# Optimization experiments

Hardware: AMD Instinct MI355X
Metric: run time of the kernel (lower is better)

The kernel has to match this reference:

```python
import jax, jax.numpy as jnp
import numpy as np


def setup_inputs() -> dict:
    key = jax.random.key(0)
    ks = jax.random.split(key, 4)
    b, n, d, dp = 8, 4096, 256, 512
    X = jax.random.normal(ks[0], (b, n, d), dtype=jnp.float32)
    P = jax.random.normal(ks[1], (b, n, d), dtype=jnp.float32)
    # linear hypernetwork params (Kaiming-ish scale)
    Wh1 = jax.random.normal(ks[2], (d, dp), dtype=jnp.float32) * (1.0 / np.sqrt(d))
    Wh2 = jax.random.normal(ks[3], (d, dp), dtype=jnp.float32) * (1.0 / np.sqrt(d))
    bh1 = jnp.zeros((dp,), dtype=jnp.float32)
    bh2 = jnp.zeros((dp,), dtype=jnp.float32)
    return {"X": X, "P": P, "Wh1": Wh1, "bh1": bh1, "Wh2": Wh2, "bh2": bh2}


def reference(X, P, Wh1, bh1, Wh2, bh2):
    # X, P: [b, n, d]
    Xp = X + P
    # hypernetwork-generated per-sample mixing weights: [b, n, d_prime]
    W1 = Xp @ Wh1 + bh1
    W2 = Xp @ Wh2 + bh2
    # token mixing: project tokens down to d_prime "mixing" space, GELU, back up
    Pm = jnp.einsum('bnp,bnd->bpd', W1, Xp)           # [b, d_prime, d]
    A = jax.nn.gelu(Pm, approximate=False)             # torch nn.GELU is exact erf form
    Y = jnp.einsum('bnp,bpd->bnd', W2, A)              # [b, n, d]
    return Y
```

## Files before the change

kernel.cpp:

```cpp
#include <hip/hip_runtime.h>

#define DEV static __device__ __forceinline__

typedef unsigned short u16;
typedef __bf16 bf16_t;
typedef __bf16 bf16x8 __attribute__((ext_vector_type(8)));
typedef float f32x4 __attribute__((ext_vector_type(4)));
typedef u16 u16x8 __attribute__((ext_vector_type(8)));

static constexpr int Bb = 8;
static constexpr int Nn = 4096;
static constexpr int Dd = 256;
static constexpr int DP = 512;

DEV void gload16(const void* g, void* l) {
  __builtin_amdgcn_global_load_lds(
      (__attribute__((address_space(1))) void*)(unsigned long long)(g),
      (__attribute__((address_space(3))) void*)(unsigned)(unsigned long long)(l),
      16, 0, 0);
}

DEV u16 f2bf(float x) { bf16_t h = (bf16_t)x; return __builtin_bit_cast(u16, h); }
DEV float bf2f(u16 v) { unsigned u = ((unsigned)v) << 16; return __builtin_bit_cast(float, u); }
DEV float gelu_exact(float x) { return 0.5f * x * (1.0f + erff(x * 0.70710678118654752f)); }

DEV void gemm_tile(const u16* Ag, int lda, const u16* Bg, int ldb,
                   int k0, int ksteps, u16* ldsA, u16* ldsB, f32x4 acc[4][4]) {
  const int tid  = threadIdx.x;
  const int wave = tid >> 6, lane = tid & 63;
  const int wr = wave >> 1, wc = wave & 1;
  const int lr = lane & 15, lk = (lane >> 4) * 8;
  const int srow = lane >> 2;
  const int skb  = (lane & 3) * 8;
  const int c0 = wave * 2, c1 = c0 + 1;
  const size_t ga0 = (size_t)(c0 * 16 + srow) * lda + skb;
  const size_t ga1 = (size_t)(c1 * 16 + srow) * lda + skb;
  const size_t gb0 = (size_t)(c0 * 16 + srow) * ldb + skb;
  const size_t gb1 = (size_t)(c1 * 16 + srow) * ldb + skb;
  u16* la0 = ldsA + c0 * 512; u16* la1 = ldsA + c1 * 512;
  u16* lb0 = ldsB + c0 * 512; u16* lb1 = ldsB + c1 * 512;

  gload16(Ag + ga0 + k0, la0); gload16(Ag + ga1 + k0, la1);
  gload16(Bg + gb0 + k0, lb0); gload16(Bg + gb1 + k0, lb1);
  asm volatile("s_waitcnt vmcnt(0)" ::: "memory");
  __syncthreads();

  int cur = 0;
  for (int kt = 0; kt < ksteps; ++kt) {
    const int nbuf = cur ^ 1;
    if (kt + 1 < ksteps) {
      const int kk = k0 + (kt + 1) * 32;
      gload16(Ag + ga0 + kk, la0 + nbuf * 4096);
      gload16(Ag + ga1 + kk, la1 + nbuf * 4096);
      gload16(Bg + gb0 + kk, lb0 + nbuf * 4096);
      gload16(Bg + gb1 + kk, lb1 + nbuf * 4096);
    }
    const u16* pa = ldsA + cur * 4096;
    const u16* pb = ldsB + cur * 4096;
    bf16x8 af[4], bfr[4];
#pragma unroll
    for (int m = 0; m < 4; ++m)
      af[m] = *(const bf16x8*)(pa + (wr * 64 + m * 16 + lr) * 32 + lk);
#pragma unroll
    for (int n = 0; n < 4; ++n)
      bfr[n] = *(const bf16x8*)(pb + (wc * 64 + n * 16 + lr) * 32 + lk);
#pragma unroll
    for (int m = 0; m < 4; ++m)
#pragma unroll
      for (int n = 0; n < 4; ++n)
        acc[m][n] = __builtin_amdgcn_mfma_f32_16x16x32_bf16(af[m], bfr[n], acc[m][n], 0, 0, 0);
    asm volatile("s_waitcnt vmcnt(0)" ::: "memory");
    __syncthreads();
    cur = nbuf;
  }
}

DEV void acc_zero(f32x4 acc[4][4]) {
#pragma unroll
  for (int m = 0; m < 4; ++m)
#pragma unroll
    for (int n = 0; n < 4; ++n) {
      f32x4 z = {0.f, 0.f, 0.f, 0.f};
      acc[m][n] = z;
    }
}

__global__ __launch_bounds__(256) void k_s1(const float* __restrict__ X, const float* __restrict__ P,
                                            const float* __restrict__ Wh1, const float* __restrict__ Wh2,
                                            u16* __restrict__ Xp, u16* __restrict__ XpT,
                                            float* __restrict__ s_part,
                                            u16* __restrict__ WhT1, u16* __restrict__ Wbf2) {
  __shared__ u16 lt[64 * 65];
  const int bid = blockIdx.x;
  const int t = threadIdx.x;
  if (bid < 2048) {
    const int b  = bid >> 8;
    const int nt = (bid >> 2) & 63;
    const int dt = bid & 3;
    const int n0 = nt * 64, d0 = dt * 64;
    const int r = t >> 2, c0 = (t & 3) * 16;
    const size_t gbase = ((size_t)(b * Nn + n0 + r)) * Dd + d0 + c0;
    u16x8 lo, hi;
#pragma unroll
    for (int i = 0; i < 4; ++i) {
      float4 xv = *(const float4*)(X + gbase + i * 4);
      float4 pv = *(const float4*)(P + gbase + i * 4);
      u16 a0 = f2bf(xv.x + pv.x), a1 = f2bf(xv.y + pv.y);
      u16 a2 = f2bf(xv.z + pv.z), a3 = f2bf(xv.w + pv.w);
      if (i < 2) { lo[i*4+0]=a0; lo[i*4+1]=a1; lo[i*4+2]=a2; lo[i*4+3]=a3; }
      else       { int q=(i-2)*4; hi[q+0]=a0; hi[q+1]=a1; hi[q+2]=a2; hi[q+3]=a3; }
      lt[r * 65 + c0 + i*4 + 0] = a0; lt[r * 65 + c0 + i*4 + 1] = a1;
      lt[r * 65 + c0 + i*4 + 2] = a2; lt[r * 65 + c0 + i*4 + 3] = a3;
    }
    *(u16x8*)(Xp + gbase)     = lo;
    *(u16x8*)(Xp + gbase + 8) = hi;
    __syncthreads();
    const int dd = t >> 2, nc0 = (t & 3) * 16;
    u16x8 olo, ohi;
    float colsum = 0.f;
#pragma unroll
    for (int i = 0; i < 8; ++i) { olo[i] = lt[(nc0 + i) * 65 + dd]; colsum += bf2f(olo[i]); }
#pragma unroll
    for (int i = 0; i < 8; ++i) { ohi[i] = lt[(nc0 + 8 + i) * 65 + dd]; colsum += bf2f(ohi[i]); }
    const size_t obase = ((size_t)(b * Dd + d0 + dd)) * Nn + n0 + nc0;
    *(u16x8*)(XpT + obase)     = olo;
    *(u16x8*)(XpT + obase + 8) = ohi;
    colsum += __shfl_xor(colsum, 1);
    colsum += __shfl_xor(colsum, 2);
    if ((t & 3) == 0) s_part[(size_t)(b * 64 + nt) * Dd + d0 + dd] = colsum;
  } else if (bid < 2048 + 32) {
    const int wb = bid - 2048;
    const int rt = (wb >> 3) & 3;
    const int ct = wb & 7;
    const int r0 = rt * 64, c0t = ct * 64;
    const int r = t >> 2, c0 = (t & 3) * 16;
    const size_t gbase = (size_t)(r0 + r) * DP + c0t + c0;
#pragma unroll
    for (int i = 0; i < 4; ++i) {
      float4 v = *(const float4*)(Wh1 + gbase + i * 4);
      lt[r * 65 + c0 + i*4 + 0] = f2bf(v.x); lt[r * 65 + c0 + i*4 + 1] = f2bf(v.y);
      lt[r * 65 + c0 + i*4 + 2] = f2bf(v.z); lt[r * 65 + c0 + i*4 + 3] = f2bf(v.w);
    }
    __syncthreads();
    const int pp = t >> 2, dc0 = (t & 3) * 16;
    u16x8 olo, ohi;
#pragma unroll
    for (int i = 0; i < 8; ++i) olo[i] = lt[(dc0 + i) * 65 + pp];
#pragma unroll
    for (int i = 0; i < 8; ++i) ohi[i] = lt[(dc0 + 8 + i) * 65 + pp];
    u16* out = WhT1 + (size_t)(c0t + pp) * Dd + r0 + dc0;
    *(u16x8*)(out)     = olo;
    *(u16x8*)(out + 8) = ohi;
  } else {
    const int idx = ((bid - 2048 - 32) * 256 + t) * 8;
    float4 v0 = *(const float4*)(Wh2 + idx);
    float4 v1 = *(const float4*)(Wh2 + idx + 4);
    u16x8 o;
    o[0]=f2bf(v0.x); o[1]=f2bf(v0.y); o[2]=f2bf(v0.z); o[3]=f2bf(v0.w);
    o[4]=f2bf(v1.x); o[5]=f2bf(v1.y); o[6]=f2bf(v1.z); o[7]=f2bf(v1.w);
    *(u16x8*)(Wbf2 + idx) = o;
  }
}

__global__ __launch_bounds__(256) void k_gram(const u16* __restrict__ XpT, float* __restrict__ G_part) {
  __shared__ __align__(16) u16 ldsA[2 * 128 * 32];
  __shared__ __align__(16) u16 ldsB[2 * 128 * 32];
  const int bid0 = blockIdx.x;
  const int bid = (bid0 & 7) * 32 + (bid0 >> 3);
  const int kc = bid & 7;
  const int tn = (bid >> 3) & 1;
  const int tm = (bid >> 4) & 1;
  const int b  = bid >> 5;
  const u16* Ag = XpT + (size_t)(b * Dd + tm * 128) * Nn;
  const u16* Bg = XpT + (size_t)(b * Dd + tn * 128) * Nn;
  f32x4 acc[4][4];
  acc_zero(acc);
  gemm_tile(Ag, Nn, Bg, Nn, kc * 512, 16, ldsA, ldsB, acc);
  const int tid = threadIdx.x, wave = tid >> 6, lane = tid & 63;
  const int wr = wave >> 1, wc = wave & 1, lr = lane & 15, lq = lane >> 4;
  float* base = G_part + (size_t)kc * (Bb * Dd * Dd) + (size_t)(b * Dd + tm * 128) * Dd + tn * 128;
#pragma unroll
  for (int m = 0; m < 4; ++m)
#pragma unroll
    for (int n = 0; n < 4; ++n)
#pragma unroll
      for (int j = 0; j < 4; ++j)
        base[(size_t)(wr * 64 + m * 16 + lq * 4 + j) * Dd + wc * 64 + n * 16 + lr] = acc[m][n][j];
}

__global__ __launch_bounds__(256) void k_gsum(const float* __restrict__ G_part,
                                              const float* __restrict__ s_part,
                                              u16* __restrict__ Gb, float* __restrict__ s,
                                              float* __restrict__ c) {
  const int bid = blockIdx.x;
  const int t = threadIdx.x;
  if (bid < 8) {
    const int b = bid, d = t;
    float sum = 0.f;
#pragma unroll 8
    for (int nt = 0; nt < 64; ++nt) sum += s_part[(size_t)(b * 64 + nt) * Dd + d];
    s[b * Dd + d] = sum;
    c[b * Dd + d] = 0.f;
  } else {
    const int e = ((bid - 8) * 256 + t) * 8;
    float4 a0 = {0.f,0.f,0.f,0.f}, a1 = {0.f,0.f,0.f,0.f};
#pragma unroll
    for (int k = 0; k < 8; ++k) {
      const float* sp = G_part + (size_t)k * (Bb * Dd * Dd) + e;
      float4 v0 = *(const float4*)(sp);
      float4 v1 = *(const float4*)(sp + 4);
      a0.x += v0.x; a0.y += v0.y; a0.z += v0.z; a0.w += v0.w;
      a1.x += v1.x; a1.y += v1.y; a1.z += v1.z; a1.w += v1.w;
    }
    u16x8 o;
    o[0]=f2bf(a0.x); o[1]=f2bf(a0.y); o[2]=f2bf(a0.z); o[3]=f2bf(a0.w);
    o[4]=f2bf(a1.x); o[5]=f2bf(a1.y); o[6]=f2bf(a1.z); o[7]=f2bf(a1.w);
    *(u16x8*)(Gb + e) = o;
  }
}

__global__ __launch_bounds__(256) void k_pmAT(const u16* __restrict__ WhT1, const u16* __restrict__ Gb,
                                              const float* __restrict__ bh1, const float* __restrict__ s,
                                              const float* __restrict__ bh2,
                                              u16* __restrict__ AT, float* __restrict__ c) {
  __shared__ __align__(16) u16 ldsA[2 * 128 * 32];
  __shared__ __align__(16) u16 ldsB[2 * 128 * 32];
  __shared__ __align__(16) u16 ct[128 * 136];
  const int bid = blockIdx.x;
  const int tn = bid & 1;
  const int tm = (bid >> 1) & 3;
  const int b  = bid >> 3;
  const int p0 = tm * 128, d0 = tn * 128;
  const u16* Ag = WhT1 + (size_t)p0 * Dd;
  const u16* Bg = Gb + (size_t)(b * Dd + d0) * Dd;
  f32x4 acc[4][4];
  acc_zero(acc);
  gemm_tile(Ag, Dd, Bg, Dd, 0, Dd / 32, ldsA, ldsB, acc);
  const int tid = threadIdx.x, wave = tid >> 6, lane = tid & 63;
  const int wr = wave >> 1, wc = wave & 1, lr = lane & 15, lq = lane >> 4;
#pragma unroll
  for (int n = 0; n < 4; ++n) {
    const int col = wc * 64 + n * 16 + lr;
    const float sv = s[b * Dd + d0 + col];
#pragma unroll
    for (int m = 0; m < 4; ++m) {
#pragma unroll
      for (int j = 0; j < 4; ++j) {
        const int row = wr * 64 + m * 16 + lq * 4 + j;
        const float pm = acc[m][n][j] + bh1[p0 + row] * sv;
        ct[col * 136 + row] = f2bf(gelu_exact(pm));
      }
    }
  }
  __syncthreads();
#pragma unroll
  for (int it = 0; it < 8; ++it) {
    const int id = tid + it * 256;
    const int dl = id >> 4, ch = id & 15;
    *(u16x8*)(AT + (size_t)(b * Dd + d0 + dl) * DP + p0 + ch * 8) =
        *(const u16x8*)(ct + dl * 136 + ch * 8);
  }
  const int ccol = tid >> 1;
  const int chalf = tid & 1;
  float csum = 0.f;
#pragma unroll
  for (int q = 0; q < 8; ++q) {
    u16x8 av = *(const u16x8*)(ct + ccol * 136 + chalf * 64 + q * 8);
#pragma unroll
    for (int i = 0; i < 8; ++i) csum += bh2[p0 + chalf * 64 + q * 8 + i] * bf2f(av[i]);
  }
  csum += __shfl_xor(csum, 1);
  if (chalf == 0) atomicAdd(c + b * Dd + d0 + ccol, csum);
}

__global__ __launch_bounds__(256) void k_h(const u16* __restrict__ Wbf2, const u16* __restrict__ AT,
                                           u16* __restrict__ HT) {
  __shared__ __align__(16) u16 ldsA[2 * 128 * 32];
  __shared__ __align__(16) u16 ldsB[2 * 128 * 32];
  __shared__ __align__(16) u16 ct[128 * 136];
  const int bid = blockIdx.x;
  const int tn = bid & 1;
  const int tm = (bid >> 1) & 1;
  const int b  = bid >> 2;
  const int k0 = tm * 128, d0 = tn * 128;
  const u16* Ag = Wbf2 + (size_t)k0 * DP;
  const u16* Bg = AT + (size_t)(b * Dd + d0) * DP;
  f32x4 acc[4][4];
  acc_zero(acc);
  gemm_tile(Ag, DP, Bg, DP, 0, DP / 32, ldsA, ldsB, acc);
  const int tid = threadIdx.x, wave = tid >> 6, lane = tid & 63;
  const int wr = wave >> 1, wc = wave & 1, lr = lane & 15, lq = lane >> 4;
#pragma unroll
  for (int n = 0; n < 4; ++n) {
    const int col = wc * 64 + n * 16 + lr;
#pragma unroll
    for (int m = 0; m < 4; ++m)
#pragma unroll
      for (int j = 0; j < 4; ++j)
        ct[col * 136 + wr * 64 + m * 16 + lq * 4 + j] = f2bf(acc[m][n][j]);
  }
  __syncthreads();
#pragma unroll
  for (int it = 0; it < 8; ++it) {
    const int id = tid + it * 256;
    const int dl = id >> 4, ch = id & 15;
    *(u16x8*)(HT + (size_t)(b * Dd + d0 + dl) * Dd + k0 + ch * 8) =
        *(const u16x8*)(ct + dl * 136 + ch * 8);
  }
}

__global__ __launch_bounds__(256) void k_y(const u16* __restrict__ Xp, const u16* __restrict__ HT,
                                           const float* __restrict__ c, float* __restrict__ Y) {
  __shared__ __align__(16) u16 ldsA[2 * 128 * 32];
  __shared__ __align__(16) u16 ldsB[2 * 128 * 32];
  const int bid0 = blockIdx.x;
  const int bid = (bid0 & 7) * 64 + (bid0 >> 3);
  const int tn = bid & 1;
  const int tm = (bid >> 1) & 31;
  const int b  = bid >> 6;
  const u16* Ag = Xp + (size_t)(b * Nn + tm * 128) * Dd;
  const u16* Bg = HT + (size_t)(b * Dd + tn * 128) * Dd;
  f32x4 acc[4][4];
  acc_zero(acc);
  gemm_tile(Ag, Dd, Bg, Dd, 0, Dd / 32, ldsA, ldsB, acc);
  const int tid = threadIdx.x, wave = tid >> 6, lane = tid & 63;
  const int wr = wave >> 1, wc = wave & 1, lr = lane & 15, lq = lane >> 4;
  float* base = Y + (size_t)(b * Nn + tm * 128) * Dd + tn * 128;
#pragma unroll
  for (int n = 0; n < 4; ++n) {
    const int col = wc * 64 + n * 16 + lr;
    const float cv = c[b * Dd + tn * 128 + col];
#pragma unroll
    for (int m = 0; m < 4; ++m)
#pragma unroll
      for (int j = 0; j < 4; ++j)
        base[(size_t)(wr * 64 + m * 16 + lq * 4 + j) * Dd + col] = acc[m][n][j] + cv;
  }
}

extern "C" void kernel_launch(void* const* d_in, const int* in_sizes, int n_in,
                              void* d_out, int out_size, void* d_ws, size_t ws_size,
                              hipStream_t stream) {
  const float* X   = (const float*)d_in[0];
  const float* P   = (const float*)d_in[1];
  const float* Wh1 = (const float*)d_in[2];
  const float* bh1 = (const float*)d_in[3];
  const float* Wh2 = (const float*)d_in[4];
  const float* bh2 = (const float*)d_in[5];
  float* Y = (float*)d_out;
  char* ws = (char*)d_ws;

  u16*   Xp     = (u16*)(ws);
  u16*   XpT    = (u16*)(ws + 16777216);
  u16*   WhT1   = (u16*)(ws + 33554432);
  u16*   Wbf2   = (u16*)(ws + 33816576);
  float* G_part = (float*)(ws + 34078720);
  float* s_part = (float*)(ws + 50855936);
  float* s      = (float*)(ws + 51380224);
  float* c      = (float*)(ws + 51388416);
  u16*   Gb     = (u16*)(ws + 51396608);
  u16*   AT     = (u16*)(ws + 52445184);
  u16*   HT     = (u16*)(ws + 54542336);
  const size_t WS_NEED = 55590912;
  if (ws_size < WS_NEED) return;

  k_s1  <<<2144, 256, 0, stream>>>(X, P, Wh1, Wh2, Xp, XpT, s_part, WhT1, Wbf2);
  k_gram<<<256,  256, 0, stream>>>(XpT, G_part);
  k_gsum<<<264,  256, 0, stream>>>(G_part, s_part, Gb, s, c);
  k_pmAT<<<64,   256, 0, stream>>>(WhT1, Gb, bh1, s, bh2, AT, c);
  k_h   <<<32,   256, 0, stream>>>(Wbf2, AT, HT);
  k_y   <<<512,  256, 0, stream>>>(Xp, HT, c, Y);
}
```

Measured before the change: 74.44 us.

## Replace split-K Gram partials and reduction kernel with atomic accumulation into fp32 G

The Gram kernel now accumulates its split-K results straight into a single fp32 G buffer with atomicAdd, and G is zeroed by extra blocks in the first kernel. This removes the separate k_gsum kernel and the 16 MB partial buffer round trip. k_pmAT reads the fp32 G directly, converts it to bf16 while loading fragments, and reduces s_part itself. It drops a launch and a lot of memory traffic, but adds atomic contention, makes the sum order nondeterministic, and uses a simpler single-buffered load loop in k_pmAT.

```diff
diff --git a/kernel.cpp b/kernel.cpp
--- a/kernel.cpp
+++ b/kernel.cpp
@@ -89,7 +89,8 @@
                                             const float* __restrict__ Wh1, const float* __restrict__ Wh2,
                                             u16* __restrict__ Xp, u16* __restrict__ XpT,
                                             float* __restrict__ s_part,
-                                            u16* __restrict__ WhT1, u16* __restrict__ Wbf2) {
+                                            u16* __restrict__ WhT1, u16* __restrict__ Wbf2,
+                                            float* __restrict__ G) {
   __shared__ u16 lt[64 * 65];
   const int bid = blockIdx.x;
   const int t = threadIdx.x;
@@ -151,7 +152,7 @@
     u16* out = WhT1 + (size_t)(c0t + pp) * Dd + r0 + dc0;
     *(u16x8*)(out)     = olo;
     *(u16x8*)(out + 8) = ohi;
-  } else {
+  } else if (bid < 2048 + 32 + 64) {
     const int idx = ((bid - 2048 - 32) * 256 + t) * 8;
     float4 v0 = *(const float4*)(Wh2 + idx);
     float4 v1 = *(const float4*)(Wh2 + idx + 4);
@@ -159,13 +160,24 @@
     o[0]=f2bf(v0.x); o[1]=f2bf(v0.y); o[2]=f2bf(v0.z); o[3]=f2bf(v0.w);
     o[4]=f2bf(v1.x); o[5]=f2bf(v1.y); o[6]=f2bf(v1.z); o[7]=f2bf(v1.w);
     *(u16x8*)(Wbf2 + idx) = o;
-  }
-}
-
-__global__ __launch_bounds__(256) void k_gram(const u16* __restrict__ XpT, float* __restrict__ G_part) {
+  } else {
+    const int idx = ((bid - 2144) * 256 + t) * 8;
+    float4 z = {0.f, 0.f, 0.f, 0.f};
+    *(float4*)(G + idx)     = z;
+    *(float4*)(G + idx + 4) = z;
+  }
+}
+
+__global__ __launch_bounds__(256) void k_gram(const u16* __restrict__ XpT, float* __restrict__ G,
+                                              float* __restrict__ c) {
   __shared__ __align__(16) u16 ldsA[2 * 128 * 32];
   __shared__ __align__(16) u16 ldsB[2 * 128 * 32];
   const int bid0 = blockIdx.x;
+  const int tid = threadIdx.x;
+  if (bid0 >= 256) {
+    c[(bid0 - 256) * Dd + tid] = 0.f;
+    return;
+  }
   const int bid = (bid0 & 7) * 32 + (bid0 >> 3);
   const int kc = bid & 7;
   const int tn = (bid >> 3) & 1;
@@ -176,78 +188,95 @@
   f32x4 acc[4][4];
   acc_zero(acc);
   gemm_tile(Ag, Nn, Bg, Nn, kc * 512, 16, ldsA, ldsB, acc);
-  const int tid = threadIdx.x, wave = tid >> 6, lane = tid & 63;
+  const int wave = tid >> 6, lane = tid & 63;
   const int wr = wave >> 1, wc = wave & 1, lr = lane & 15, lq = lane >> 4;
-  float* base = G_part + (size_t)kc * (Bb * Dd * Dd) + (size_t)(b * Dd + tm * 128) * Dd + tn * 128;
+  float* base = G + (size_t)(b * Dd + tm * 128) * Dd + tn * 128;
 #pragma unroll
   for (int m = 0; m < 4; ++m)
 #pragma unroll
     for (int n = 0; n < 4; ++n)
 #pragma unroll
       for (int j = 0; j < 4; ++j)
-        base[(size_t)(wr * 64 + m * 16 + lq * 4 + j) * Dd + wc * 64 + n * 16 + lr] = acc[m][n][j];
-}
-
-__global__ __launch_bounds__(256) void k_gsum(const float* __restrict__ G_part,
+        atomicAdd(base + (size_t)(wr * 64 + m * 16 + lq * 4 + j) * Dd + wc * 64 + n * 16 + lr,
+                  acc[m][n][j]);
+}
+
+__global__ __launch_bounds__(256) void k_pmAT(const u16* __restrict__ WhT1, const float* __restrict__ G,
                                               const float* __restrict__ s_part,
-                                              u16* __restrict__ Gb, float* __restrict__ s,
-                                              float* __restrict__ c) {
-  const int bid = blockIdx.x;
-  const int t = threadIdx.x;
-  if (bid < 8) {
-    const int b = bid, d = t;
-    float sum = 0.f;
-#pragma unroll 8
-    for (int nt = 0; nt < 64; ++nt) sum += s_part[(size_t)(b * 64 + nt) * Dd + d];
-    s[b * Dd + d] = sum;
-    c[b * Dd + d] = 0.f;
-  } else {
-    const int e = ((bid - 8) * 256 + t) * 8;
-    float4 a0 = {0.f,0.f,0.f,0.f}, a1 = {0.f,0.f,0.f,0.f};
-#pragma unroll
-    for (int k = 0; k < 8; ++k) {
-      const float* sp = G_part + (size_t)k * (Bb * Dd * Dd) + e;
-      float4 v0 = *(const float4*)(sp);
-      float4 v1 = *(const float4*)(sp + 4);
-      a0.x += v0.x; a0.y += v0.y; a0.z += v0.z; a0.w += v0.w;
-      a1.x += v1.x; a1.y += v1.y; a1.z += v1.z; a1.w += v1.w;
-    }
-    u16x8 o;
-    o[0]=f2bf(a0.x); o[1]=f2bf(a0.y); o[2]=f2bf(a0.z); o[3]=f2bf(a0.w);
-    o[4]=f2bf(a1.x); o[5]=f2bf(a1.y); o[6]=f2bf(a1.z); o[7]=f2bf(a1.w);
-    *(u16x8*)(Gb + e) = o;
-  }
-}
-
-__global__ __launch_bounds__(256) void k_pmAT(const u16* __restrict__ WhT1, const u16* __restrict__ Gb,
-                                              const float* __restrict__ bh1, const float* __restrict__ s,
-                                              const float* __restrict__ bh2,
+                                              const float* __restrict__ bh1, const float* __restrict__ bh2,
                                               u16* __restrict__ AT, float* __restrict__ c) {
-  __shared__ __align__(16) u16 ldsA[2 * 128 * 32];
-  __shared__ __align__(16) u16 ldsB[2 * 128 * 32];
+  __shared__ __align__(16) u16 ldsA[128 * 32];
+  __shared__ __align__(16) float ldsBf[128 * 32];
   __shared__ __align__(16) u16 ct[128 * 136];
+  __shared__ float sv[128];
   const int bid = blockIdx.x;
   const int tn = bid & 1;
   const int tm = (bid >> 1) & 3;
   const int b  = bid >> 3;
   const int p0 = tm * 128, d0 = tn * 128;
-  const u16* Ag = WhT1 + (size_t)p0 * Dd;
-  const u16* Bg = Gb + (size_t)(b * Dd + d0) * Dd;
+  const int tid = threadIdx.x;
+  const int wave = tid >> 6, lane = tid & 63;
+  const int wr = wave >> 1, wc = wave & 1, lr = lane & 15, lq = lane >> 4;
+  const int lk = lq * 8;
+
+  if (tid < 128) {
+    float sum = 0.f;
+#pragma unroll 8
+    for (int nt = 0; nt < 64; ++nt) sum += s_part[(size_t)(b * 64 + nt) * Dd + d0 + tid];
+    sv[tid] = sum;
+  }
+
+  const u16*   Ag = WhT1 + (size_t)p0 * Dd;
+  const float* Bg = G + (size_t)(b * Dd + d0) * Dd;
+
+  const int srowA = lane >> 2, skbA = (lane & 3) * 8;
+  const int srowB = lane >> 3, skbB = (lane & 7) * 4;
+  const int c0 = wave * 2, c1 = c0 + 1;
+
   f32x4 acc[4][4];
   acc_zero(acc);
-  gemm_tile(Ag, Dd, Bg, Dd, 0, Dd / 32, ldsA, ldsB, acc);
-  const int tid = threadIdx.x, wave = tid >> 6, lane = tid & 63;
-  const int wr = wave >> 1, wc = wave & 1, lr = lane & 15, lq = lane >> 4;
+  for (int kt = 0; kt < 8; ++kt) {
+    const int kk = kt * 32;
+    gload16(Ag + (size_t)(c0 * 16 + srowA) * Dd + kk + skbA, ldsA + c0 * 512);
+    gload16(Ag + (size_t)(c1 * 16 + srowA) * Dd + kk + skbA, ldsA + c1 * 512);
+    gload16(Bg + (size_t)(c0 * 16 + srowB) * Dd + kk + skbB, ldsBf + c0 * 512);
+    gload16(Bg + (size_t)(c0 * 16 + 8 + srowB) * Dd + kk + skbB, ldsBf + c0 * 512 + 256);
+    gload16(Bg + (size_t)(c1 * 16 + srowB) * Dd + kk + skbB, ldsBf + c1 * 512);
+    gload16(Bg + (size_t)(c1 * 16 + 8 + srowB) * Dd + kk + skbB, ldsBf + c1 * 512 + 256);
+    asm volatile("s_waitcnt vmcnt(0)" ::: "memory");
+    __syncthreads();
+    bf16x8 af[4], bfr[4];
+#pragma unroll
+    for (int m = 0; m < 4; ++m)
+      af[m] = *(const bf16x8*)(ldsA + (wr * 64 + m * 16 + lr) * 32 + lk);
+#pragma unroll
+    for (int n = 0; n < 4; ++n) {
+      const float* bp = ldsBf + (wc * 64 + n * 16 + lr) * 32 + lk;
+      float4 v0 = *(const float4*)(bp);
+      float4 v1 = *(const float4*)(bp + 4);
+      bf16x8 f;
+      f[0]=(bf16_t)v0.x; f[1]=(bf16_t)v0.y; f[2]=(bf16_t)v0.z; f[3]=(bf16_t)v0.w;
+      f[4]=(bf16_t)v1.x; f[5]=(bf16_t)v1.y; f[6]=(bf16_t)v1.z; f[7]=(bf16_t)v1.w;
+      bfr[n] = f;
+    }
+#pragma unroll
+    for (int m = 0; m < 4; ++m)
+#pragma unroll
+      for (int n = 0; n < 4; ++n)
+        acc[m][n] = __builtin_amdgcn_mfma_f32_16x16x32_bf16(af[m], bfr[n], acc[m][n], 0, 0, 0);
+    __syncthreads();
+  }
+
 #pragma unroll
   for (int n = 0; n < 4; ++n) {
     const int col = wc * 64 + n * 16 + lr;
-    const float sv = s[b * Dd + d0 + col];
+    const float svv = sv[col];
 #pragma unroll
     for (int m = 0; m < 4; ++m) {
 #pragma unroll
       for (int j = 0; j < 4; ++j) {
         const int row = wr * 64 + m * 16 + lq * 4 + j;
-        const float pm = acc[m][n][j] + bh1[p0 + row] * sv;
+        const float pm = acc[m][n][j] + bh1[p0 + row] * svv;
         ct[col * 136 + row] = f2bf(gelu_exact(pm));
       }
     }
@@ -354,20 +383,17 @@
   u16*   XpT    = (u16*)(ws + 16777216);
   u16*   WhT1   = (u16*)(ws + 33554432);
   u16*   Wbf2   = (u16*)(ws + 33816576);
-  float* G_part = (float*)(ws + 34078720);
-  float* s_part = (float*)(ws + 50855936);
-  float* s      = (float*)(ws + 51380224);
-  float* c      = (float*)(ws + 51388416);
-  u16*   Gb     = (u16*)(ws + 51396608);
-  u16*   AT     = (u16*)(ws + 52445184);
-  u16*   HT     = (u16*)(ws + 54542336);
-  const size_t WS_NEED = 55590912;
+  float* G      = (float*)(ws + 34078720);
+  float* s_part = (float*)(ws + 36175872);
+  float* c      = (float*)(ws + 36700160);
+  u16*   AT     = (u16*)(ws + 36708352);
+  u16*   HT     = (u16*)(ws + 38805504);
+  const size_t WS_NEED = 39854080;
   if (ws_size < WS_NEED) return;
 
-  k_s1  <<<2144, 256, 0, stream>>>(X, P, Wh1, Wh2, Xp, XpT, s_part, WhT1, Wbf2);
-  k_gram<<<256,  256, 0, stream>>>(XpT, G_part);
-  k_gsum<<<264,  256, 0, stream>>>(G_part, s_part, Gb, s, c);
-  k_pmAT<<<64,   256, 0, stream>>>(WhT1, Gb, bh1, s, bh2, AT, c);
+  k_s1  <<<2400, 256, 0, stream>>>(X, P, Wh1, Wh2, Xp, XpT, s_part, WhT1, Wbf2, G);
+  k_gram<<<264,  256, 0, stream>>>(XpT, G, c);
+  k_pmAT<<<64,   256, 0, stream>>>(WhT1, G, s_part, bh1, bh2, AT, c);
   k_h   <<<32,   256, 0, stream>>>(Wbf2, AT, HT);
   k_y   <<<512,  256, 0, stream>>>(Xp, HT, c, Y);
 }
```

Result: slower. 91.99 us (+23.6%).

## Halve N-tile width for gram and Y GEMMs; store gram partials in bf16

Applied to the files above, without the earlier changes.

Templates the shared GEMM tile on its N width so k_gram and k_y use 128x64 tiles, doubling their grids (512 and 1024 blocks) to fill more compute units on the MI355X. The gram split-K partials are now stored as bf16 instead of fp32, halving the partial buffer traffic written by k_gram and read by k_gsum. The trade-off is less data reuse per tile (A is reloaded twice as often) and extra rounding of partial sums before the reduction.

```diff
diff --git a/kernel.cpp b/kernel.cpp
--- a/kernel.cpp
+++ b/kernel.cpp
@@ -24,24 +24,33 @@
 DEV float bf2f(u16 v) { unsigned u = ((unsigned)v) << 16; return __builtin_bit_cast(float, u); }
 DEV float gelu_exact(float x) { return 0.5f * x * (1.0f + erff(x * 0.70710678118654752f)); }
 
+template <int NT>
 DEV void gemm_tile(const u16* Ag, int lda, const u16* Bg, int ldb,
-                   int k0, int ksteps, u16* ldsA, u16* ldsB, f32x4 acc[4][4]) {
+                   int k0, int ksteps, u16* ldsA, u16* ldsB, f32x4 acc[4][NT]) {
   const int tid  = threadIdx.x;
   const int wave = tid >> 6, lane = tid & 63;
   const int wr = wave >> 1, wc = wave & 1;
   const int lr = lane & 15, lk = (lane >> 4) * 8;
   const int srow = lane >> 2;
   const int skb  = (lane & 3) * 8;
-  const int c0 = wave * 2, c1 = c0 + 1;
-  const size_t ga0 = (size_t)(c0 * 16 + srow) * lda + skb;
-  const size_t ga1 = (size_t)(c1 * 16 + srow) * lda + skb;
-  const size_t gb0 = (size_t)(c0 * 16 + srow) * ldb + skb;
-  const size_t gb1 = (size_t)(c1 * 16 + srow) * ldb + skb;
-  u16* la0 = ldsA + c0 * 512; u16* la1 = ldsA + c1 * 512;
-  u16* lb0 = ldsB + c0 * 512; u16* lb1 = ldsB + c1 * 512;
+  constexpr int BCH = NT / 2;
+  constexpr int BBUF = NT * 1024;
+
+  const int ca0 = wave * 2, ca1 = ca0 + 1;
+  const size_t ga0 = (size_t)(ca0 * 16 + srow) * lda + skb;
+  const size_t ga1 = (size_t)(ca1 * 16 + srow) * lda + skb;
+  u16* la0 = ldsA + ca0 * 512; u16* la1 = ldsA + ca1 * 512;
+  size_t gb[BCH]; u16* lb[BCH];
+#pragma unroll
+  for (int i = 0; i < BCH; ++i) {
+    const int ch = wave * BCH + i;
+    gb[i] = (size_t)(ch * 16 + srow) * ldb + skb;
+    lb[i] = ldsB + ch * 512;
+  }
 
   gload16(Ag + ga0 + k0, la0); gload16(Ag + ga1 + k0, la1);
-  gload16(Bg + gb0 + k0, lb0); gload16(Bg + gb1 + k0, lb1);
+#pragma unroll
+  for (int i = 0; i < BCH; ++i) gload16(Bg + gb[i] + k0, lb[i]);
   asm volatile("s_waitcnt vmcnt(0)" ::: "memory");
   __syncthreads();
 
@@ -52,22 +61,22 @@
       const int kk = k0 + (kt + 1) * 32;
       gload16(Ag + ga0 + kk, la0 + nbuf * 4096);
       gload16(Ag + ga1 + kk, la1 + nbuf * 4096);
-      gload16(Bg + gb0 + kk, lb0 + nbuf * 4096);
-      gload16(Bg + gb1 + kk, lb1 + nbuf * 4096);
+#pragma unroll
+      for (int i = 0; i < BCH; ++i) gload16(Bg + gb[i] + kk, lb[i] + nbuf * BBUF);
     }
     const u16* pa = ldsA + cur * 4096;
-    const u16* pb = ldsB + cur * 4096;
-    bf16x8 af[4], bfr[4];
+    const u16* pb = ldsB + cur * BBUF;
+    bf16x8 af[4], bfr[NT];
 #pragma unroll
     for (int m = 0; m < 4; ++m)
       af[m] = *(const bf16x8*)(pa + (wr * 64 + m * 16 + lr) * 32 + lk);
 #pragma unroll
-    for (int n = 0; n < 4; ++n)
-      bfr[n] = *(const bf16x8*)(pb + (wc * 64 + n * 16 + lr) * 32 + lk);
+    for (int n = 0; n < NT; ++n)
+      bfr[n] = *(const bf16x8*)(pb + (wc * (NT * 16) + n * 16 + lr) * 32 + lk);
 #pragma unroll
     for (int m = 0; m < 4; ++m)
 #pragma unroll
-      for (int n = 0; n < 4; ++n)
+      for (int n = 0; n < NT; ++n)
         acc[m][n] = __builtin_amdgcn_mfma_f32_16x16x32_bf16(af[m], bfr[n], acc[m][n], 0, 0, 0);
     asm volatile("s_waitcnt vmcnt(0)" ::: "memory");
     __syncthreads();
@@ -75,11 +84,12 @@
   }
 }
 
-DEV void acc_zero(f32x4 acc[4][4]) {
+template <int NT>
+DEV void acc_zero(f32x4 acc[4][NT]) {
 #pragma unroll
   for (int m = 0; m < 4; ++m)
 #pragma unroll
-    for (int n = 0; n < 4; ++n) {
+    for (int n = 0; n < NT; ++n) {
       f32x4 z = {0.f, 0.f, 0.f, 0.f};
       acc[m][n] = z;
     }
@@ -162,33 +172,34 @@
   }
 }
 
-__global__ __launch_bounds__(256) void k_gram(const u16* __restrict__ XpT, float* __restrict__ G_part) {
+__global__ __launch_bounds__(256) void k_gram(const u16* __restrict__ XpT, u16* __restrict__ G_part) {
   __shared__ __align__(16) u16 ldsA[2 * 128 * 32];
-  __shared__ __align__(16) u16 ldsB[2 * 128 * 32];
+  __shared__ __align__(16) u16 ldsB[2 * 64 * 32];
   const int bid0 = blockIdx.x;
-  const int bid = (bid0 & 7) * 32 + (bid0 >> 3);
+  const int bid = (bid0 & 7) * 64 + (bid0 >> 3);
   const int kc = bid & 7;
-  const int tn = (bid >> 3) & 1;
-  const int tm = (bid >> 4) & 1;
-  const int b  = bid >> 5;
+  const int tn = (bid >> 3) & 3;
+  const int tm = (bid >> 5) & 1;
+  const int b  = bid >> 6;
   const u16* Ag = XpT + (size_t)(b * Dd + tm * 128) * Nn;
-  const u16* Bg = XpT + (size_t)(b * Dd + tn * 128) * Nn;
-  f32x4 acc[4][4];
-  acc_zero(acc);
-  gemm_tile(Ag, Nn, Bg, Nn, kc * 512, 16, ldsA, ldsB, acc);
+  const u16* Bg = XpT + (size_t)(b * Dd + tn * 64) * Nn;
+  f32x4 acc[4][2];
+  acc_zero<2>(acc);
+  gemm_tile<2>(Ag, Nn, Bg, Nn, kc * 512, 16, ldsA, ldsB, acc);
   const int tid = threadIdx.x, wave = tid >> 6, lane = tid & 63;
   const int wr = wave >> 1, wc = wave & 1, lr = lane & 15, lq = lane >> 4;
-  float* base = G_part + (size_t)kc * (Bb * Dd * Dd) + (size_t)(b * Dd + tm * 128) * Dd + tn * 128;
+  u16* base = G_part + (size_t)kc * (Bb * Dd * Dd) + (size_t)(b * Dd + tm * 128) * Dd + tn * 64;
 #pragma unroll
   for (int m = 0; m < 4; ++m)
 #pragma unroll
-    for (int n = 0; n < 4; ++n)
+    for (int n = 0; n < 2; ++n)
 #pragma unroll
       for (int j = 0; j < 4; ++j)
-        base[(size_t)(wr * 64 + m * 16 + lq * 4 + j) * Dd + wc * 64 + n * 16 + lr] = acc[m][n][j];
-}
-
-__global__ __launch_bounds__(256) void k_gsum(const float* __restrict__ G_part,
+        base[(size_t)(wr * 64 + m * 16 + lq * 4 + j) * Dd + wc * 32 + n * 16 + lr] =
+            f2bf(acc[m][n][j]);
+}
+
+__global__ __launch_bounds__(256) void k_gsum(const u16* __restrict__ G_part,
                                               const float* __restrict__ s_part,
                                               u16* __restrict__ Gb, float* __restrict__ s,
                                               float* __restrict__ c) {
@@ -203,18 +214,16 @@
     c[b * Dd + d] = 0.f;
   } else {
     const int e = ((bid - 8) * 256 + t) * 8;
-    float4 a0 = {0.f,0.f,0.f,0.f}, a1 = {0.f,0.f,0.f,0.f};
+    float a[8] = {0.f,0.f,0.f,0.f,0.f,0.f,0.f,0.f};
 #pragma unroll
     for (int k = 0; k < 8; ++k) {
-      const float* sp = G_part + (size_t)k * (Bb * Dd * Dd) + e;
-      float4 v0 = *(const float4*)(sp);
-      float4 v1 = *(const float4*)(sp + 4);
-      a0.x += v0.x; a0.y += v0.y; a0.z += v0.z; a0.w += v0.w;
-      a1.x += v1.x; a1.y += v1.y; a1.z += v1.z; a1.w += v1.w;
+      u16x8 v = *(const u16x8*)(G_part + (size_t)k * (Bb * Dd * Dd) + e);
+#pragma unroll
+      for (int i = 0; i < 8; ++i) a[i] += bf2f(v[i]);
     }
     u16x8 o;
-    o[0]=f2bf(a0.x); o[1]=f2bf(a0.y); o[2]=f2bf(a0.z); o[3]=f2bf(a0.w);
-    o[4]=f2bf(a1.x); o[5]=f2bf(a1.y); o[6]=f2bf(a1.z); o[7]=f2bf(a1.w);
+#pragma unroll
+    for (int i = 0; i < 8; ++i) o[i] = f2bf(a[i]);
     *(u16x8*)(Gb + e) = o;
   }
 }
@@ -234,8 +243,8 @@
   const u16* Ag = WhT1 + (size_t)p0 * Dd;
   const u16* Bg = Gb + (size_t)(b * Dd + d0) * Dd;
   f32x4 acc[4][4];
-  acc_zero(acc);
-  gemm_tile(Ag, Dd, Bg, Dd, 0, Dd / 32, ldsA, ldsB, acc);
+  acc_zero<4>(acc);
+  gemm_tile<4>(Ag, Dd, Bg, Dd, 0, Dd / 32, ldsA, ldsB, acc);
   const int tid = threadIdx.x, wave = tid >> 6, lane = tid & 63;
   const int wr = wave >> 1, wc = wave & 1, lr = lane & 15, lq = lane >> 4;
 #pragma unroll
@@ -286,8 +295,8 @@
   const u16* Ag = Wbf2 + (size_t)k0 * DP;
   const u16* Bg = AT + (size_t)(b * Dd + d0) * DP;
   f32x4 acc[4][4];
-  acc_zero(acc);
-  gemm_tile(Ag, DP, Bg, DP, 0, DP / 32, ldsA, ldsB, acc);
+  acc_zero<4>(acc);
+  gemm_tile<4>(Ag, DP, Bg, DP, 0, DP / 32, ldsA, ldsB, acc);
   const int tid = threadIdx.x, wave = tid >> 6, lane = tid & 63;
   const int wr = wave >> 1, wc = wave & 1, lr = lane & 15, lq = lane >> 4;
 #pragma unroll
@@ -312,24 +321,24 @@
 __global__ __launch_bounds__(256) void k_y(const u16* __restrict__ Xp, const u16* __restrict__ HT,
                                            const float* __restrict__ c, float* __restrict__ Y) {
   __shared__ __align__(16) u16 ldsA[2 * 128 * 32];
-  __shared__ __align__(16) u16 ldsB[2 * 128 * 32];
+  __shared__ __align__(16) u16 ldsB[2 * 64 * 32];
   const int bid0 = blockIdx.x;
-  const int bid = (bid0 & 7) * 64 + (bid0 >> 3);
-  const int tn = bid & 1;
-  const int tm = (bid >> 1) & 31;
-  const int b  = bid >> 6;
+  const int bid = (bid0 & 7) * 128 + (bid0 >> 3);
+  const int b  = bid >> 7;
+  const int tm = (bid >> 2) & 31;
+  const int tn = bid & 3;
   const u16* Ag = Xp + (size_t)(b * Nn + tm * 128) * Dd;
-  const u16* Bg = HT + (size_t)(b * Dd + tn * 128) * Dd;
-  f32x4 acc[4][4];
-  acc_zero(acc);
-  gemm_tile(Ag, Dd, Bg, Dd, 0, Dd / 32, ldsA, ldsB, acc);
+  const u16* Bg = HT + (size_t)(b * Dd + tn * 64) * Dd;
+  f32x4 acc[4][2];
+  acc_zero<2>(acc);
+  gemm_tile<2>(Ag, Dd, Bg, Dd, 0, Dd / 32, ldsA, ldsB, acc);
   const int tid = threadIdx.x, wave = tid >> 6, lane = tid & 63;
   const int wr = wave >> 1, wc = wave & 1, lr = lane & 15, lq = lane >> 4;
-  float* base = Y + (size_t)(b * Nn + tm * 128) * Dd + tn * 128;
-#pragma unroll
-  for (int n = 0; n < 4; ++n) {
-    const int col = wc * 64 + n * 16 + lr;
-    const float cv = c[b * Dd + tn * 128 + col];
+  float* base = Y + (size_t)(b * Nn + tm * 128) * Dd + tn * 64;
+#pragma unroll
+  for (int n = 0; n < 2; ++n) {
+    const int col = wc * 32 + n * 16 + lr;
+    const float cv = c[b * Dd + tn * 64 + col];
 #pragma unroll
     for (int m = 0; m < 4; ++m)
 #pragma unroll
@@ -354,20 +363,20 @@
   u16*   XpT    = (u16*)(ws + 16777216);
   u16*   WhT1   = (u16*)(ws + 33554432);
   u16*   Wbf2   = (u16*)(ws + 33816576);
-  float* G_part = (float*)(ws + 34078720);
-  float* s_part = (float*)(ws + 50855936);
-  float* s      = (float*)(ws + 51380224);
-  float* c      = (float*)(ws + 51388416);
-  u16*   Gb     = (u16*)(ws + 51396608);
-  u16*   AT     = (u16*)(ws + 52445184);
-  u16*   HT     = (u16*)(ws + 54542336);
-  const size_t WS_NEED = 55590912;
+  u16*   G_part = (u16*)(ws + 34078720);
+  float* s_part = (float*)(ws + 42467328);
+  float* s      = (float*)(ws + 42991616);
+  float* c      = (float*)(ws + 42999808);
+  u16*   Gb     = (u16*)(ws + 43008000);
+  u16*   AT     = (u16*)(ws + 44056576);
+  u16*   HT     = (u16*)(ws + 46153728);
+  const size_t WS_NEED = 47202304;
   if (ws_size < WS_NEED) return;
 
   k_s1  <<<2144, 256, 0, stream>>>(X, P, Wh1, Wh2, Xp, XpT, s_part, WhT1, Wbf2);
-  k_gram<<<256,  256, 0, stream>>>(XpT, G_part);
+  k_gram<<<512,  256, 0, stream>>>(XpT, G_part);
   k_gsum<<<264,  256, 0, stream>>>(G_part, s_part, Gb, s, c);
   k_pmAT<<<64,   256, 0, stream>>>(WhT1, Gb, bh1, s, bh2, AT, c);
   k_h   <<<32,   256, 0, stream>>>(Wbf2, AT, HT);
-  k_y   <<<512,  256, 0, stream>>>(Xp, HT, c, Y);
-}
+  k_y   <<<1024, 256, 0, stream>>>(Xp, HT, c, Y);
+}
```

Measured after the change: 72.14 us. -3.1%, faster.
